# Kernel optimization log

Hardware: AMD Instinct MI355X
Metric: run time of the kernel (lower is better)

Reference implementation:

```python
import jax, jax.numpy as jnp
import numpy as np

B, N, D = 64, 2048, 256
EPS = 1e-05


def setup_inputs() -> dict:
    key = jax.random.key(0)
    k1, k2 = jax.random.split(key)
    x = jax.random.normal(k1, (B, N, D), dtype=jnp.float32)
    lengths = jax.random.randint(k2, (B,), 1, N + 1, dtype=jnp.int32)
    weights = jnp.ones((D,), dtype=jnp.float32)
    biases = jnp.zeros((D,), dtype=jnp.float32)
    return {"x": x, "lengths": lengths, "weights": weights, "biases": biases}


def reference(x, lengths, weights, biases):
    # mask: [B, N, 1], 1.0 for valid set elements (idx < length)
    mask = (jnp.arange(N)[None, :] < lengths[:, None])[..., None].astype(x.dtype)
    denom = (lengths.astype(x.dtype) * D)  # [B]
    xm = x * mask
    means = jnp.sum(xm, axis=(1, 2)) / denom                      # [B]
    x_centered = (xm - means[:, None, None]) * mask               # [B,N,D]
    variances = jnp.sum(x_centered * x_centered, axis=(1, 2)) / denom  # [B]
    x_norm = x_centered / (jnp.sqrt(variances)[:, None, None] + EPS)
    # F.linear(x, diag_embed(w), b) == x * w + b (elementwise per-feature affine)
    out = (x_norm * weights + biases) * mask
    return out
```

## Files before the change

kernel.cpp:

```cpp
#include <hip/hip_runtime.h>


#define BB 64
#define NN 2048
#define DD 256
#define EPSV 1e-5f
#define CHUNKS 32
#define ROWS_PER_CHUNK (NN / CHUNKS)

typedef float f32x4 __attribute__((ext_vector_type(4)));

__global__ __launch_bounds__(256) void setnorm_partials(
    const float* __restrict__ x, const int* __restrict__ lengths,
    float* __restrict__ partials) {
  const int c = blockIdx.x;
  const int b = blockIdx.y;
  const int len = lengths[b];
  const int rowBase = c * ROWS_PER_CHUNK;
  int validRows = len - rowBase;
  if (validRows > ROWS_PER_CHUNK) validRows = ROWS_PER_CHUNK;

  float sum = 0.f, sumsq = 0.f;
  if (validRows > 0) {
    const f32x4* p =
        (const f32x4*)(x + ((size_t)b * NN + (size_t)rowBase) * DD);
    const int n4 = validRows * (DD / 4);
    for (int i = threadIdx.x; i < n4; i += 512) {
      f32x4 v = p[i];
      sum += v.x + v.y + v.z + v.w;
      sumsq += v.x * v.x + v.y * v.y + v.z * v.z + v.w * v.w;
      const int j = i + 256;
      if (j < n4) {
        f32x4 u = p[j];
        sum += u.x + u.y + u.z + u.w;
        sumsq += u.x * u.x + u.y * u.y + u.z * u.z + u.w * u.w;
      }
    }
  }
  #pragma unroll
  for (int off = 32; off > 0; off >>= 1) {
    sum += __shfl_down(sum, off, 64);
    sumsq += __shfl_down(sumsq, off, 64);
  }
  __shared__ float ssum[4], ssq[4];
  const int wave = threadIdx.x >> 6;
  const int lane = threadIdx.x & 63;
  if (lane == 0) { ssum[wave] = sum; ssq[wave] = sumsq; }
  __syncthreads();
  if (threadIdx.x == 0) {
    float ts = 0.f, tq = 0.f;
    #pragma unroll
    for (int w = 0; w < 4; ++w) { ts += ssum[w]; tq += ssq[w]; }
    partials[(b * CHUNKS + c) * 2 + 0] = ts;
    partials[(b * CHUNKS + c) * 2 + 1] = tq;
  }
}

__global__ __launch_bounds__(256) void setnorm_norm(
    const float* __restrict__ x, const int* __restrict__ lengths,
    const float* __restrict__ weights, const float* __restrict__ biases,
    const float* __restrict__ partials, float* __restrict__ out) {
  const int blockBase = blockIdx.x * 1024;
  const int b = blockBase >> 17;
  const int row0 = (blockBase & 131071) >> 6;
  const int len = lengths[b];

  if (row0 >= len) {
    const f32x4 z = {0.f, 0.f, 0.f, 0.f};
    #pragma unroll
    for (int i = 0; i < 4; ++i)
      __builtin_nontemporal_store(z,
          ((f32x4*)out) + blockBase + i * 256 + threadIdx.x);
    return;
  }

  __shared__ float s_mean, s_inv;
  if (threadIdx.x < 64) {
    float s = 0.f, q = 0.f;
    if (threadIdx.x < CHUNKS) {
      s = partials[(b * CHUNKS + threadIdx.x) * 2 + 0];
      q = partials[(b * CHUNKS + threadIdx.x) * 2 + 1];
    }
    #pragma unroll
    for (int off = 16; off > 0; off >>= 1) {
      s += __shfl_down(s, off, 64);
      q += __shfl_down(q, off, 64);
    }
    if (threadIdx.x == 0) {
      const float denom = (float)lengths[b] * (float)DD;
      const float mean = s / denom;
      float var = q / denom - mean * mean;
      var = fmaxf(var, 0.f);
      s_mean = mean;
      s_inv = 1.f / (sqrtf(var) + EPSV);
    }
  }
  __syncthreads();
  const float mean = s_mean;
  const float inv = s_inv;

  const int d4 = threadIdx.x & 63;
  const f32x4 w = ((const f32x4*)weights)[d4];
  const f32x4 bi = ((const f32x4*)biases)[d4];
  const int rowT = row0 + (threadIdx.x >> 6);

  #pragma unroll
  for (int i = 0; i < 4; ++i) {
    const int idx4 = blockBase + i * 256 + threadIdx.x;
    const int row = rowT + i * 4;
    f32x4 o = {0.f, 0.f, 0.f, 0.f};
    if (row < len) {
      const f32x4 v = ((const f32x4*)x)[idx4];
      o.x = (v.x - mean) * inv * w.x + bi.x;
      o.y = (v.y - mean) * inv * w.y + bi.y;
      o.z = (v.z - mean) * inv * w.z + bi.z;
      o.w = (v.w - mean) * inv * w.w + bi.w;
    }
    __builtin_nontemporal_store(o, ((f32x4*)out) + idx4);
  }
}

extern "C" void kernel_launch(void* const* d_in, const int* in_sizes, int n_in,
                              void* d_out, int out_size, void* d_ws, size_t ws_size,
                              hipStream_t stream) {
  const float* x = (const float*)d_in[0];
  const int* lengths = (const int*)d_in[1];
  const float* weights = (const float*)d_in[2];
  const float* biases = (const float*)d_in[3];
  float* out = (float*)d_out;

  float* partials = (float*)d_ws;

  dim3 g1(CHUNKS, BB);
  setnorm_partials<<<g1, 256, 0, stream>>>(x, lengths, partials);
  const int total4 = BB * NN * DD / 4;
  setnorm_norm<<<total4 / 1024, 256, 0, stream>>>(x, lengths, weights, biases,
                                                  partials, out);
}
```

Before: 230.1 us.

## Fuse stats and normalize passes into one cooperative kernel with grid sync

Replaces the two-kernel approach (partial sums, then normalize) with a single cooperative kernel. Each block reduces its 128-row slice, the whole grid synchronizes, and the same block then normalizes its slice, so the second read of x is more likely to hit in L2/MALL. This removes one kernel launch and keeps each block's data local. In exchange it adds a grid-wide barrier, caps the grid at 1024 resident blocks, and gives each block 128 rows in both phases, which may cause load imbalance from variable lengths.

```diff
diff --git a/kernel.cpp b/kernel.cpp
--- a/kernel.cpp
+++ b/kernel.cpp
@@ -1,37 +1,41 @@
 #include <hip/hip_runtime.h>
+#include <hip/hip_cooperative_groups.h>
 
+
+namespace cg = cooperative_groups;
 
 #define BB 64
 #define NN 2048
 #define DD 256
 #define EPSV 1e-5f
-#define CHUNKS 32
-#define ROWS_PER_CHUNK (NN / CHUNKS)
+#define BPB 16
+#define ROWS_PER_BLOCK (NN / BPB)
+#define GRID_BLOCKS (BB * BPB)
 
 typedef float f32x4 __attribute__((ext_vector_type(4)));
 
-__global__ __launch_bounds__(256) void setnorm_partials(
+__global__ __launch_bounds__(256, 4) void setnorm_fused(
     const float* __restrict__ x, const int* __restrict__ lengths,
-    float* __restrict__ partials) {
-  const int c = blockIdx.x;
-  const int b = blockIdx.y;
+    const float* __restrict__ weights, const float* __restrict__ biases,
+    float* __restrict__ partials, float* __restrict__ out) {
+  const int slice = blockIdx.x & (BPB - 1);
+  const int b = blockIdx.x >> 4;
   const int len = lengths[b];
-  const int rowBase = c * ROWS_PER_CHUNK;
-  int validRows = len - rowBase;
-  if (validRows > ROWS_PER_CHUNK) validRows = ROWS_PER_CHUNK;
+  const int rowBase = slice * ROWS_PER_BLOCK;
 
   float sum = 0.f, sumsq = 0.f;
+  int validRows = len - rowBase;
+  if (validRows > ROWS_PER_BLOCK) validRows = ROWS_PER_BLOCK;
+  const f32x4* xs = (const f32x4*)(x + ((size_t)b * NN + (size_t)rowBase) * DD);
   if (validRows > 0) {
-    const f32x4* p =
-        (const f32x4*)(x + ((size_t)b * NN + (size_t)rowBase) * DD);
     const int n4 = validRows * (DD / 4);
     for (int i = threadIdx.x; i < n4; i += 512) {
-      f32x4 v = p[i];
+      f32x4 v = xs[i];
       sum += v.x + v.y + v.z + v.w;
       sumsq += v.x * v.x + v.y * v.y + v.z * v.z + v.w * v.w;
       const int j = i + 256;
       if (j < n4) {
-        f32x4 u = p[j];
+        f32x4 u = xs[j];
         sum += u.x + u.y + u.z + u.w;
         sumsq += u.x * u.x + u.y * u.y + u.z * u.z + u.w * u.w;
       }
@@ -51,43 +55,36 @@
     float ts = 0.f, tq = 0.f;
     #pragma unroll
     for (int w = 0; w < 4; ++w) { ts += ssum[w]; tq += ssq[w]; }
-    partials[(b * CHUNKS + c) * 2 + 0] = ts;
-    partials[(b * CHUNKS + c) * 2 + 1] = tq;
+    partials[(b * BPB + slice) * 2 + 0] = ts;
+    partials[(b * BPB + slice) * 2 + 1] = tq;
   }
-}
 
-__global__ __launch_bounds__(256) void setnorm_norm(
-    const float* __restrict__ x, const int* __restrict__ lengths,
-    const float* __restrict__ weights, const float* __restrict__ biases,
-    const float* __restrict__ partials, float* __restrict__ out) {
-  const int blockBase = blockIdx.x * 1024;
-  const int b = blockBase >> 17;
-  const int row0 = (blockBase & 131071) >> 6;
-  const int len = lengths[b];
+  cg::this_grid().sync();
 
-  if (row0 >= len) {
+  f32x4* op = ((f32x4*)out) + ((size_t)b * NN + (size_t)rowBase) * (DD / 4);
+
+  if (rowBase >= len) {
     const f32x4 z = {0.f, 0.f, 0.f, 0.f};
     #pragma unroll
-    for (int i = 0; i < 4; ++i)
-      __builtin_nontemporal_store(z,
-          ((f32x4*)out) + blockBase + i * 256 + threadIdx.x);
+    for (int i = 0; i < 32; ++i)
+      __builtin_nontemporal_store(z, op + i * 256 + threadIdx.x);
     return;
   }
 
   __shared__ float s_mean, s_inv;
   if (threadIdx.x < 64) {
     float s = 0.f, q = 0.f;
-    if (threadIdx.x < CHUNKS) {
-      s = partials[(b * CHUNKS + threadIdx.x) * 2 + 0];
-      q = partials[(b * CHUNKS + threadIdx.x) * 2 + 1];
+    if (threadIdx.x < BPB) {
+      s = partials[(b * BPB + threadIdx.x) * 2 + 0];
+      q = partials[(b * BPB + threadIdx.x) * 2 + 1];
     }
     #pragma unroll
-    for (int off = 16; off > 0; off >>= 1) {
+    for (int off = 8; off > 0; off >>= 1) {
       s += __shfl_down(s, off, 64);
       q += __shfl_down(q, off, 64);
     }
     if (threadIdx.x == 0) {
-      const float denom = (float)lengths[b] * (float)DD;
+      const float denom = (float)len * (float)DD;
       const float mean = s / denom;
       float var = q / denom - mean * mean;
       var = fmaxf(var, 0.f);
@@ -102,21 +99,21 @@
   const int d4 = threadIdx.x & 63;
   const f32x4 w = ((const f32x4*)weights)[d4];
   const f32x4 bi = ((const f32x4*)biases)[d4];
-  const int rowT = row0 + (threadIdx.x >> 6);
+  const int rowT = rowBase + (threadIdx.x >> 6);
 
-  #pragma unroll
-  for (int i = 0; i < 4; ++i) {
-    const int idx4 = blockBase + i * 256 + threadIdx.x;
+  #pragma unroll 4
+  for (int i = 0; i < 32; ++i) {
+    const int o4 = i * 256 + threadIdx.x;
     const int row = rowT + i * 4;
     f32x4 o = {0.f, 0.f, 0.f, 0.f};
     if (row < len) {
-      const f32x4 v = ((const f32x4*)x)[idx4];
+      const f32x4 v = xs[o4];
       o.x = (v.x - mean) * inv * w.x + bi.x;
       o.y = (v.y - mean) * inv * w.y + bi.y;
       o.z = (v.z - mean) * inv * w.z + bi.z;
       o.w = (v.w - mean) * inv * w.w + bi.w;
     }
-    __builtin_nontemporal_store(o, ((f32x4*)out) + idx4);
+    __builtin_nontemporal_store(o, op + o4);
   }
 }
 
@@ -128,12 +125,10 @@
   const float* weights = (const float*)d_in[2];
   const float* biases = (const float*)d_in[3];
   float* out = (float*)d_out;
-
   float* partials = (float*)d_ws;
 
-  dim3 g1(CHUNKS, BB);
-  setnorm_partials<<<g1, 256, 0, stream>>>(x, lengths, partials);
-  const int total4 = BB * NN * DD / 4;
-  setnorm_norm<<<total4 / 1024, 256, 0, stream>>>(x, lengths, weights, biases,
-                                                  partials, out);
+  void* args[] = {(void*)&x, (void*)&lengths, (void*)&weights,
+                  (void*)&biases, (void*)&partials, (void*)&out};
+  hipLaunchCooperativeKernel((void*)setnorm_fused, dim3(GRID_BLOCKS),
+                             dim3(256), args, 0, stream);
 }
```

Result: slower. 345.5 us (+50.2%).
